# Performance work log

Measured on AMD Instinct MI355X. Metric: run time of the kernel, lower is better.

Reference implementation:

```python
import jax, jax.numpy as jnp
import numpy as np

SIGMAS = [0.5, 1.0, 2.0, 4.0, 8.0]
FILTER_SIZE = int(4 * SIGMAS[-1] + 1)  # 33
PAD = int(2 * SIGMAS[-1])              # 16
K1, K2 = 0.01, 0.03
ALPHA = 0.025
COMPENSATION = 20.0
DATA_RANGE = 1.0


def _gauss_2d(size, sigma):
    coords = np.arange(size, dtype=np.float32) - size // 2
    g = np.exp(-coords ** 2 / (2.0 * sigma ** 2))
    g = g / g.sum()
    return np.outer(g, g)


def _build_g_masks():
    # [n_sigmas, 1, 33, 33] OIHW
    masks = np.stack([_gauss_2d(FILTER_SIZE, s)[None] for s in SIGMAS], axis=0)
    return jnp.asarray(masks, dtype=jnp.float32)


def setup_inputs() -> dict:
    key = jax.random.key(0)
    kx, ky = jax.random.split(key)
    x = jax.random.uniform(kx, (16, 1, 512, 512), dtype=jnp.float32)
    y = jax.random.uniform(ky, (16, 1, 512, 512), dtype=jnp.float32)
    return {"x": x, "y": y, "g_masks": _build_g_masks()}


def _conv(t, w):
    # t: [B,1,H,W], w: [O,1,33,33] -> [B,O,H,W] ('same' padding)
    return jax.lax.conv_general_dilated(
        t, w, window_strides=(1, 1), padding=[(PAD, PAD), (PAD, PAD)],
        dimension_numbers=("NCHW", "OIHW", "NCHW"))


def reference(x, y, g_masks):
    C1 = (K1 * DATA_RANGE) ** 2
    C2 = (K2 * DATA_RANGE) ** 2

    mux = _conv(x, g_masks)   # [B,5,H,W]
    muy = _conv(y, g_masks)
    mux2 = mux * mux
    muy2 = muy * muy
    muxy = mux * muy
    sigmax2 = _conv(x * x, g_masks) - mux2
    sigmay2 = _conv(y * y, g_masks) - muy2
    sigmaxy = _conv(x * y, g_masks) - muxy

    luminance = (2.0 * muxy + C1) / (mux2 + muy2 + C1)
    cs = (2.0 * sigmaxy + C2) / (sigmax2 + sigmay2 + C2)

    lM = luminance[:, -1, :, :]          # largest-scale luminance
    PIcs = jnp.prod(cs, axis=1)          # product of contrast-structure over scales
    loss_ms_ssim = 1.0 - lM * PIcs       # [B,H,W]

    loss_l1 = jnp.abs(x - y)             # [B,1,H,W]
    gaussian_l1 = _conv(loss_l1, g_masks[-1:]).mean(axis=1)  # [B,H,W]

    loss_mix = ALPHA * loss_ms_ssim + (1.0 - ALPHA) * gaussian_l1 / DATA_RANGE
    return (COMPENSATION * loss_mix).mean()
```

## Files before the change

### kernel.cpp

```cpp
#include <hip/hip_runtime.h>
#include <hip/hip_bf16.h>

namespace {

constexpr float kAlpha = 0.025f;
constexpr float kC1 = 1.0e-4f;
constexpr float kC2 = 9.0e-4f;

constexpr int MPS = 68;
constexpr int HTS = 68;

typedef __attribute__((ext_vector_type(8))) short short8;
typedef __attribute__((ext_vector_type(4))) float f32x4;

struct __align__(16) Smem {
  union {
    short mp[2][64 * MPS];
    short hbT[8][32 * HTS];
  };
  float red[4];
  int gtab[2][5][48];
};

union Frag {
  int i[4];
  short8 s8;
};

__device__ __forceinline__ unsigned f2bf(float f) {
  unsigned u = __float_as_uint(f);
  return (u + 0x7FFFu + ((u >> 16) & 1u)) >> 16;
}
__device__ __forceinline__ unsigned pk(float a, float b) {
  union {
    __hip_bfloat162 h;
    unsigned u;
  } c;
  c.h = __float22bfloat162_rn(make_float2(a, b));
  return c.u;
}
__device__ __forceinline__ float bfl(unsigned u) {
  return __uint_as_float(u << 16);
}
__device__ __forceinline__ float bfh(unsigned u) {
  return __uint_as_float(u & 0xFFFF0000u);
}
__device__ __forceinline__ float frcp(float x) {
  return __builtin_amdgcn_rcpf(x);
}

__device__ __forceinline__ short8 wbuild2(const int* tb, int nt, int kt) {
  Frag u;
#pragma unroll
  for (int j = 0; j < 4; ++j) u.i[j] = tb[16 * kt - 8 * nt + 8 + j];
  return u.s8;
}

__device__ __forceinline__ void load_xy(const Smem& sm, int row, int quad,
                                        Frag fx[2], Frag fy[2]) {
  const short* px = &sm.mp[0][row * MPS + quad * 8];
  const short* py = &sm.mp[1][row * MPS + quad * 8];
  *(int2*)&fx[0].i[0] = *(const int2*)(px);
  *(int2*)&fx[0].i[2] = *(const int2*)(px + 4);
  *(int2*)&fx[1].i[0] = *(const int2*)(px + 32);
  *(int2*)&fx[1].i[2] = *(const int2*)(px + 36);
  *(int2*)&fy[0].i[0] = *(const int2*)(py);
  *(int2*)&fy[0].i[2] = *(const int2*)(py + 4);
  *(int2*)&fy[1].i[0] = *(const int2*)(py + 32);
  *(int2*)&fy[1].i[2] = *(const int2*)(py + 36);
}

__global__ __launch_bounds__(256, 2) void msssim_l1_kernel(
    const float* __restrict__ x, const float* __restrict__ y,
    const float* __restrict__ gm, float* __restrict__ out) {
  __shared__ Smem sm;
  const int tid = threadIdx.x;
  const int lane = tid & 63;
  const int w = tid >> 6;
  const int quad = lane >> 4;
  const int l16 = lane & 15;

  float corr;
  {
    float traw4 = (lane < 33) ? gm[4 * 1089 + 528 + lane] : 0.f;
    float g = traw4 * rsqrtf(__shfl(traw4, 16, 64));
    float se = g, st = bfl(f2bf(g));
#pragma unroll
    for (int off = 32; off > 0; off >>= 1) {
      se += __shfl_xor(se, off, 64);
      st += __shfl_xor(st, off, 64);
    }
    float r1 = se / st;
    corr = r1 * r1;
  }

  {
    int* gt = &sm.gtab[0][0][0];
    for (int q = tid; q < 480; q += 256) {
      int par = q >= 240;
      int rem = par ? q - 240 : q;
      int s = rem / 48;
      int i = rem - s * 48;
      int t0 = 2 * i + par;
      const float* grow = gm + s * 1089 + 528;
      float rsc = rsqrtf(grow[16]);
      int g0 = t0 - 31, g1 = t0 - 30;
      unsigned lo = (g0 >= 0 && g0 <= 32) ? f2bf(grow[g0] * rsc) : 0u;
      unsigned hi = (g1 >= 0 && g1 <= 32) ? f2bf(grow[g1] * rsc) : 0u;
      gt[q] = (int)(lo | (hi << 16));
    }
  }

  const int D = (quad * 8 - l16 + 31) >> 1;
  const int* gD = &sm.gtab[(l16 & 1) ? 0 : 1][0][0] + D - 8;

  const float* xb = x + blockIdx.z * (512 * 512);
  const float* yb = y + blockIdx.z * (512 * 512);
  const int rb = blockIdx.y * 32 - 16;
  const int cb = blockIdx.x * 32 - 16;
  for (int f = tid; f < 1024; f += 256) {
    int pr = f >> 4;
    int pc = (f & 15) << 2;
    int gr = rb + pr, gc = cb + pc;
    float4 vx = make_float4(0.f, 0.f, 0.f, 0.f);
    float4 vy = vx;
    if (gr >= 0 && gr < 512 && gc >= 0 && gc < 512) {
      vx = *(const float4*)(xb + gr * 512 + gc);
      vy = *(const float4*)(yb + gr * 512 + gc);
    }
    const int base = pr * MPS + pc;
    *(int2*)(&sm.mp[0][base]) =
        make_int2((int)pk(vx.x, vx.y), (int)pk(vx.z, vx.w));
    *(int2*)(&sm.mp[1][base]) =
        make_int2((int)pk(vy.x, vy.y), (int)pk(vy.z, vy.w));
  }
  __syncthreads();

  Frag A[4][2];
  Frag dA[2];
#pragma unroll
  for (int mt = 0; mt < 4; ++mt) {
    Frag fx[2], fy[2];
    load_xy(sm, mt * 16 + l16, quad, fx, fy);
    if (mt == w) {
#pragma unroll
      for (int h = 0; h < 2; ++h)
#pragma unroll
        for (int i = 0; i < 4; ++i) {
          unsigned ux = (unsigned)fx[h].i[i], uy = (unsigned)fy[h].i[i];
          dA[h].i[i] =
              (int)pk(fabsf(bfl(ux) - bfl(uy)), fabsf(bfh(ux) - bfh(uy)));
        }
    }
    if (w == 0) {
      A[mt][0] = fx[0];
      A[mt][1] = fx[1];
    } else if (w == 1) {
      A[mt][0] = fy[0];
      A[mt][1] = fy[1];
    } else {
#pragma unroll
      for (int h = 0; h < 2; ++h)
#pragma unroll
        for (int i = 0; i < 4; ++i) {
          unsigned ux = (unsigned)fx[h].i[i], uy = (unsigned)fy[h].i[i];
          float xl = bfl(ux), xh = bfh(ux), yl = bfl(uy), yh = bfh(uy);
          A[mt][h].i[i] = (w == 2) ? (int)pk(fmaf(xl, xl, yl * yl),
                                            fmaf(xh, xh, yh * yh))
                                   : (int)pk(xl * yl, xh * yh);
        }
    }
  }
  __syncthreads();

  const int mtv = w >> 1, ntv = w & 1;
  f32x4 Pcs = {1.f, 1.f, 1.f, 1.f};
  f32x4 lumP = {0.f, 0.f, 0.f, 0.f};
  f32x4 l1v = {0.f, 0.f, 0.f, 0.f};

#pragma unroll
  for (int gidx = 0; gidx < 2; ++gidx) {
    const int s0 = gidx * 2;
#pragma unroll
    for (int ds = 0; ds < 2; ++ds) {
      const int s = s0 + ds;
      const int* tb = gD + s * 48;
      short8 wf[2][2];
#pragma unroll
      for (int nt = 0; nt < 2; ++nt)
#pragma unroll
        for (int kt = 0; kt < 2; ++kt) wf[nt][kt] = wbuild2(tb, nt, kt);
#pragma unroll
      for (int mt = 0; mt < 4; ++mt)
#pragma unroll
        for (int nt = 0; nt < 2; ++nt) {
          f32x4 acc = {0.f, 0.f, 0.f, 0.f};
          acc = __builtin_amdgcn_mfma_f32_16x16x32_bf16(A[mt][0].s8, wf[nt][0],
                                                        acc, 0, 0, 0);
          acc = __builtin_amdgcn_mfma_f32_16x16x32_bf16(A[mt][1].s8, wf[nt][1],
                                                        acc, 0, 0, 0);
          *(int2*)(&sm.hbT[ds * 4 + w][(nt * 16 + l16) * HTS + mt * 16 +
                                       quad * 4]) =
              make_int2((int)pk(acc[0], acc[1]), (int)pk(acc[2], acc[3]));
        }
    }
    __syncthreads();

#pragma unroll
    for (int ds = 0; ds < 2; ++ds) {
      const int s = s0 + ds;
      const int* tb = gD + s * 48;
      short8 wa0 = wbuild2(tb, mtv, 0);
      short8 wa1 = wbuild2(tb, mtv, 1);
      f32x4 va[4];
#pragma unroll
      for (int m = 0; m < 4; ++m) {
        const short* bp =
            &sm.hbT[ds * 4 + m][(ntv * 16 + l16) * HTS + quad * 8];
        Frag b0, b1;
        *(int2*)&b0.i[0] = *(const int2*)(bp);
        *(int2*)&b0.i[2] = *(const int2*)(bp + 4);
        *(int2*)&b1.i[0] = *(const int2*)(bp + 32);
        *(int2*)&b1.i[2] = *(const int2*)(bp + 36);
        f32x4 acc = {0.f, 0.f, 0.f, 0.f};
        acc = __builtin_amdgcn_mfma_f32_16x16x32_bf16(wa0, b0.s8, acc, 0, 0,
                                                      0);
        acc = __builtin_amdgcn_mfma_f32_16x16x32_bf16(wa1, b1.s8, acc, 0, 0,
                                                      0);
        va[m] = acc;
      }
#pragma unroll
      for (int r = 0; r < 4; ++r) {
        float mux = va[0][r], muy = va[1][r], m2 = va[2][r], mxy = va[3][r];
        float cs = (2.f * (mxy - mux * muy) + kC2) *
                   frcp((m2 - mux * mux - muy * muy) + kC2);
        Pcs[r] *= cs;
      }
    }
    __syncthreads();
  }

  {
    const int* tb = gD + 4 * 48;
    short8 wf[2][2];
#pragma unroll
    for (int nt = 0; nt < 2; ++nt)
#pragma unroll
      for (int kt = 0; kt < 2; ++kt) wf[nt][kt] = wbuild2(tb, nt, kt);
#pragma unroll
    for (int mt = 0; mt < 4; ++mt)
#pragma unroll
      for (int nt = 0; nt < 2; ++nt) {
        f32x4 acc = {0.f, 0.f, 0.f, 0.f};
        acc = __builtin_amdgcn_mfma_f32_16x16x32_bf16(A[mt][0].s8, wf[nt][0],
                                                      acc, 0, 0, 0);
        acc = __builtin_amdgcn_mfma_f32_16x16x32_bf16(A[mt][1].s8, wf[nt][1],
                                                      acc, 0, 0, 0);
        *(int2*)(&sm.hbT[w][(nt * 16 + l16) * HTS + mt * 16 + quad * 4]) =
            make_int2((int)pk(acc[0], acc[1]), (int)pk(acc[2], acc[3]));
      }
#pragma unroll
    for (int nt = 0; nt < 2; ++nt) {
      f32x4 acc = {0.f, 0.f, 0.f, 0.f};
      acc = __builtin_amdgcn_mfma_f32_16x16x32_bf16(dA[0].s8, wf[nt][0], acc,
                                                    0, 0, 0);
      acc = __builtin_amdgcn_mfma_f32_16x16x32_bf16(dA[1].s8, wf[nt][1], acc,
                                                    0, 0, 0);
      *(int2*)(&sm.hbT[4][(nt * 16 + l16) * HTS + w * 16 + quad * 4]) =
          make_int2((int)pk(acc[0], acc[1]), (int)pk(acc[2], acc[3]));
    }
    __syncthreads();

    short8 wa0 = wbuild2(tb, mtv, 0);
    short8 wa1 = wbuild2(tb, mtv, 1);
    f32x4 va[5];
#pragma unroll
    for (int m = 0; m < 5; ++m) {
      const short* bp = &sm.hbT[m][(ntv * 16 + l16) * HTS + quad * 8];
      Frag b0, b1;
      *(int2*)&b0.i[0] = *(const int2*)(bp);
      *(int2*)&b0.i[2] = *(const int2*)(bp + 4);
      *(int2*)&b1.i[0] = *(const int2*)(bp + 32);
      *(int2*)&b1.i[2] = *(const int2*)(bp + 36);
      f32x4 acc = {0.f, 0.f, 0.f, 0.f};
      acc = __builtin_amdgcn_mfma_f32_16x16x32_bf16(wa0, b0.s8, acc, 0, 0, 0);
      acc = __builtin_amdgcn_mfma_f32_16x16x32_bf16(wa1, b1.s8, acc, 0, 0, 0);
      va[m] = acc;
    }
#pragma unroll
    for (int r = 0; r < 4; ++r) {
      float mux = va[0][r], muy = va[1][r], m2 = va[2][r], mxy = va[3][r];
      float mux2 = mux * mux, muy2 = muy * muy, muxy = mux * muy;
      float cs = (2.f * (mxy - muxy) + kC2) * frcp((m2 - mux2 - muy2) + kC2);
      Pcs[r] *= cs;
      lumP[r] = ((2.f * muxy + kC1) * frcp(mux2 + muy2 + kC1)) * Pcs[r];
      l1v[r] = va[4][r] * corr;
    }
  }

  float lsum = 0.f;
#pragma unroll
  for (int r = 0; r < 4; ++r)
    lsum += kAlpha * (1.f - lumP[r]) + (1.f - kAlpha) * l1v[r];
#pragma unroll
  for (int off = 32; off > 0; off >>= 1) lsum += __shfl_down(lsum, off, 64);
  if ((tid & 63) == 0) sm.red[tid >> 6] = lsum;
  __syncthreads();
  if (tid == 0) {
    float t = sm.red[0] + sm.red[1] + sm.red[2] + sm.red[3];
    atomicAdd(out, t * (20.f / (16.f * 512.f * 512.f)));
  }
}

}

extern "C" void kernel_launch(void* const* d_in, const int* in_sizes, int n_in,
                              void* d_out, int out_size, void* d_ws,
                              size_t ws_size, hipStream_t stream) {
  (void)in_sizes;
  (void)n_in;
  (void)d_ws;
  (void)ws_size;
  (void)out_size;
  const float* x = (const float*)d_in[0];
  const float* y = (const float*)d_in[1];
  const float* gm = (const float*)d_in[2];
  float* out = (float*)d_out;
  hipMemsetAsync(out, 0, sizeof(float), stream);
  dim3 grid(16, 16, 16);
  msssim_l1_kernel<<<grid, dim3(256), 0, stream>>>(x, y, gm, out);
}
```

Measured before the change: 146.2 us.

## Process one scale per pass with smaller LDS buffer and higher occupancy

Reduces the transposed intermediate LDS buffer from 8 slots to 4 by handling one Gaussian scale per pass instead of two. The L1 blur moves to a separate final pass that reuses slot 0. Launch bounds are raised from 2 to 8 blocks per CU to take advantage of the smaller shared-memory footprint. The trade-off is more __syncthreads barriers and tighter register limits under the higher occupancy target, which could cause spills.

```diff
diff --git a/kernel.cpp b/kernel.cpp
--- a/kernel.cpp
+++ b/kernel.cpp
@@ -16,7 +16,7 @@
 struct __align__(16) Smem {
   union {
     short mp[2][64 * MPS];
-    short hbT[8][32 * HTS];
+    short hbT[4][32 * HTS];
   };
   float red[4];
   int gtab[2][5][48];
@@ -70,7 +70,7 @@
   *(int2*)&fy[1].i[2] = *(const int2*)(py + 36);
 }
 
-__global__ __launch_bounds__(256, 2) void msssim_l1_kernel(
+__global__ __launch_bounds__(256, 8) void msssim_l1_kernel(
     const float* __restrict__ x, const float* __restrict__ y,
     const float* __restrict__ gm, float* __restrict__ out) {
   __shared__ Smem sm;
@@ -179,69 +179,8 @@
   f32x4 l1v = {0.f, 0.f, 0.f, 0.f};
 
 #pragma unroll
-  for (int gidx = 0; gidx < 2; ++gidx) {
-    const int s0 = gidx * 2;
-#pragma unroll
-    for (int ds = 0; ds < 2; ++ds) {
-      const int s = s0 + ds;
-      const int* tb = gD + s * 48;
-      short8 wf[2][2];
-#pragma unroll
-      for (int nt = 0; nt < 2; ++nt)
-#pragma unroll
-        for (int kt = 0; kt < 2; ++kt) wf[nt][kt] = wbuild2(tb, nt, kt);
-#pragma unroll
-      for (int mt = 0; mt < 4; ++mt)
-#pragma unroll
-        for (int nt = 0; nt < 2; ++nt) {
-          f32x4 acc = {0.f, 0.f, 0.f, 0.f};
-          acc = __builtin_amdgcn_mfma_f32_16x16x32_bf16(A[mt][0].s8, wf[nt][0],
-                                                        acc, 0, 0, 0);
-          acc = __builtin_amdgcn_mfma_f32_16x16x32_bf16(A[mt][1].s8, wf[nt][1],
-                                                        acc, 0, 0, 0);
-          *(int2*)(&sm.hbT[ds * 4 + w][(nt * 16 + l16) * HTS + mt * 16 +
-                                       quad * 4]) =
-              make_int2((int)pk(acc[0], acc[1]), (int)pk(acc[2], acc[3]));
-        }
-    }
-    __syncthreads();
-
-#pragma unroll
-    for (int ds = 0; ds < 2; ++ds) {
-      const int s = s0 + ds;
-      const int* tb = gD + s * 48;
-      short8 wa0 = wbuild2(tb, mtv, 0);
-      short8 wa1 = wbuild2(tb, mtv, 1);
-      f32x4 va[4];
-#pragma unroll
-      for (int m = 0; m < 4; ++m) {
-        const short* bp =
-            &sm.hbT[ds * 4 + m][(ntv * 16 + l16) * HTS + quad * 8];
-        Frag b0, b1;
-        *(int2*)&b0.i[0] = *(const int2*)(bp);
-        *(int2*)&b0.i[2] = *(const int2*)(bp + 4);
-        *(int2*)&b1.i[0] = *(const int2*)(bp + 32);
-        *(int2*)&b1.i[2] = *(const int2*)(bp + 36);
-        f32x4 acc = {0.f, 0.f, 0.f, 0.f};
-        acc = __builtin_amdgcn_mfma_f32_16x16x32_bf16(wa0, b0.s8, acc, 0, 0,
-                                                      0);
-        acc = __builtin_amdgcn_mfma_f32_16x16x32_bf16(wa1, b1.s8, acc, 0, 0,
-                                                      0);
-        va[m] = acc;
-      }
-#pragma unroll
-      for (int r = 0; r < 4; ++r) {
-        float mux = va[0][r], muy = va[1][r], m2 = va[2][r], mxy = va[3][r];
-        float cs = (2.f * (mxy - mux * muy) + kC2) *
-                   frcp((m2 - mux * mux - muy * muy) + kC2);
-        Pcs[r] *= cs;
-      }
-    }
-    __syncthreads();
-  }
-
-  {
-    const int* tb = gD + 4 * 48;
+  for (int s = 0; s < 5; ++s) {
+    const int* tb = gD + s * 48;
     short8 wf[2][2];
 #pragma unroll
     for (int nt = 0; nt < 2; ++nt)
@@ -259,23 +198,13 @@
         *(int2*)(&sm.hbT[w][(nt * 16 + l16) * HTS + mt * 16 + quad * 4]) =
             make_int2((int)pk(acc[0], acc[1]), (int)pk(acc[2], acc[3]));
       }
-#pragma unroll
-    for (int nt = 0; nt < 2; ++nt) {
-      f32x4 acc = {0.f, 0.f, 0.f, 0.f};
-      acc = __builtin_amdgcn_mfma_f32_16x16x32_bf16(dA[0].s8, wf[nt][0], acc,
-                                                    0, 0, 0);
-      acc = __builtin_amdgcn_mfma_f32_16x16x32_bf16(dA[1].s8, wf[nt][1], acc,
-                                                    0, 0, 0);
-      *(int2*)(&sm.hbT[4][(nt * 16 + l16) * HTS + w * 16 + quad * 4]) =
-          make_int2((int)pk(acc[0], acc[1]), (int)pk(acc[2], acc[3]));
-    }
     __syncthreads();
 
     short8 wa0 = wbuild2(tb, mtv, 0);
     short8 wa1 = wbuild2(tb, mtv, 1);
-    f32x4 va[5];
-#pragma unroll
-    for (int m = 0; m < 5; ++m) {
+    f32x4 va[4];
+#pragma unroll
+    for (int m = 0; m < 4; ++m) {
       const short* bp = &sm.hbT[m][(ntv * 16 + l16) * HTS + quad * 8];
       Frag b0, b1;
       *(int2*)&b0.i[0] = *(const int2*)(bp);
@@ -293,9 +222,44 @@
       float mux2 = mux * mux, muy2 = muy * muy, muxy = mux * muy;
       float cs = (2.f * (mxy - muxy) + kC2) * frcp((m2 - mux2 - muy2) + kC2);
       Pcs[r] *= cs;
-      lumP[r] = ((2.f * muxy + kC1) * frcp(mux2 + muy2 + kC1)) * Pcs[r];
-      l1v[r] = va[4][r] * corr;
-    }
+      if (s == 4)
+        lumP[r] = ((2.f * muxy + kC1) * frcp(mux2 + muy2 + kC1)) * Pcs[r];
+    }
+    __syncthreads();
+  }
+
+  {
+    const int* tb = gD + 4 * 48;
+    short8 wf[2][2];
+#pragma unroll
+    for (int nt = 0; nt < 2; ++nt)
+#pragma unroll
+      for (int kt = 0; kt < 2; ++kt) wf[nt][kt] = wbuild2(tb, nt, kt);
+#pragma unroll
+    for (int nt = 0; nt < 2; ++nt) {
+      f32x4 acc = {0.f, 0.f, 0.f, 0.f};
+      acc = __builtin_amdgcn_mfma_f32_16x16x32_bf16(dA[0].s8, wf[nt][0], acc,
+                                                    0, 0, 0);
+      acc = __builtin_amdgcn_mfma_f32_16x16x32_bf16(dA[1].s8, wf[nt][1], acc,
+                                                    0, 0, 0);
+      *(int2*)(&sm.hbT[0][(nt * 16 + l16) * HTS + w * 16 + quad * 4]) =
+          make_int2((int)pk(acc[0], acc[1]), (int)pk(acc[2], acc[3]));
+    }
+    __syncthreads();
+
+    short8 wa0 = wbuild2(tb, mtv, 0);
+    short8 wa1 = wbuild2(tb, mtv, 1);
+    const short* bp = &sm.hbT[0][(ntv * 16 + l16) * HTS + quad * 8];
+    Frag b0, b1;
+    *(int2*)&b0.i[0] = *(const int2*)(bp);
+    *(int2*)&b0.i[2] = *(const int2*)(bp + 4);
+    *(int2*)&b1.i[0] = *(const int2*)(bp + 32);
+    *(int2*)&b1.i[2] = *(const int2*)(bp + 36);
+    f32x4 acc = {0.f, 0.f, 0.f, 0.f};
+    acc = __builtin_amdgcn_mfma_f32_16x16x32_bf16(wa0, b0.s8, acc, 0, 0, 0);
+    acc = __builtin_amdgcn_mfma_f32_16x16x32_bf16(wa1, b1.s8, acc, 0, 0, 0);
+#pragma unroll
+    for (int r = 0; r < 4; ++r) l1v[r] = acc[r] * corr;
   }
 
   float lsum = 0.f;
```

New measurement: 178.7 us. +22.2%, slower.
